# Optimization experiments

Hardware: AMD Instinct MI355X
Metric: run time of the kernel (lower is better)

The kernel has to match this reference:

```python
import jax, jax.numpy as jnp
import numpy as np

V, E, H, L, B, T = 32000, 512, 512, 4, 32, 64

def setup_inputs() -> dict:
    key = jax.random.key(0)
    ks = jax.random.split(key, 12)
    s = 0.04  # ~1/sqrt(H), matches torch LSTMCell uniform scale magnitude
    emb = jax.random.normal(ks[0], (V, E), jnp.float32) * s
    emb = emb.at[0].set(0.0)  # padding_idx=0
    return {
        'context': jax.random.normal(ks[1], (B, T, H), jnp.float32),
        'dec_input': jax.random.randint(ks[2], (B, T), 0, V),
        'h0': jax.random.normal(ks[3], (L, B, H), jnp.float32) * s,
        'c0': jax.random.normal(ks[4], (L, B, H), jnp.float32) * s,
        'emb': emb,
        'W_ih': jax.random.normal(ks[5], (L, 4 * H, E), jnp.float32) * s,
        'W_hh': jax.random.normal(ks[6], (L, 4 * H, H), jnp.float32) * s,
        'b_ih': jax.random.normal(ks[7], (L, 4 * H), jnp.float32) * s,
        'b_hh': jax.random.normal(ks[8], (L, 4 * H), jnp.float32) * s,
        'W_cls': jax.random.normal(ks[9], (V, H), jnp.float32) * s,
        'b_cls': jax.random.normal(ks[10], (V,), jnp.float32) * s,
    }

def _stack_lstm_scan(x, h0, c0, W_ih, W_hh, b_ih, b_hh):
    # x: [B,T,E] -> scan over time with L stacked LSTMCells + residual
    n_layers = W_ih.shape[0]

    def step(carry, x_t):
        h, c = carry  # each [L,B,H]
        inp = x_t
        new_h, new_c = [], []
        for i in range(n_layers):
            gates = inp @ W_ih[i].T + b_ih[i] + h[i] @ W_hh[i].T + b_hh[i]
            ig, fg, gg, og = jnp.split(gates, 4, axis=-1)  # torch order: i,f,g,o
            ci = jax.nn.sigmoid(fg) * c[i] + jax.nn.sigmoid(ig) * jnp.tanh(gg)
            hi = jax.nn.sigmoid(og) * jnp.tanh(ci)
            # residual when dims match (E == H here)
            inp = hi + inp if inp.shape[-1] == hi.shape[-1] else hi
            new_h.append(hi)
            new_c.append(ci)
        return (jnp.stack(new_h), jnp.stack(new_c)), inp

    (hT, cT), outs = jax.lax.scan(step, (h0, c0), jnp.swapaxes(x, 0, 1))
    return jnp.swapaxes(outs, 0, 1), hT, cT  # [B,T,H]

def reference(context, dec_input, h0, c0, emb, W_ih, W_hh, b_ih, b_hh, W_cls, b_cls):
    x = emb[dec_input]  # [B,T,E]; dropouts are identity (p=0 / eval)
    outs, hT, cT = _stack_lstm_scan(x, h0, c0, W_ih, W_hh, b_ih, b_hh)
    logits = outs @ W_cls.T + b_cls  # [B,T,V]
    # original applies log_softmax over dim=1 (the sequence dim) - faithful
    out = jax.nn.log_softmax(logits, axis=1)
    return (out, hT, cT)
```

## Files before the change

kernel.cpp:

```cpp
#include <hip/hip_runtime.h>
#include <math.h>

#define VOCAB 32000
#define HDIM  512
#define NLAYERS 4
#define BATCH 32
#define TSTEPS 64
typedef unsigned long long ULL;

typedef __attribute__((ext_vector_type(8))) short bf16x8;
typedef __attribute__((ext_vector_type(4))) float f32x4;

static __device__ __forceinline__ unsigned short f2b(float f) {
    union { float f; unsigned u; } v; v.f = f;
    return (unsigned short)((v.u + 0x7FFFu + ((v.u >> 16) & 1u)) >> 16);
}
static __device__ __forceinline__ float sigf(float x) { return 1.0f / (1.0f + __expf(-x)); }

static __device__ __forceinline__ int apack_off(int m, int k) {
    int k0 = k >> 5, mi = m >> 4;
    int lane = (m & 15) | (((k >> 3) & 3) << 4);
    return ((k0 * 2 + mi) * 64 + lane) * 8 + (k & 7);
}

__global__ void k_prep_w(const float* __restrict__ W_ih, const float* __restrict__ W_hh,
                         unsigned short* __restrict__ wp) {
    const int total = NLAYERS * 64 * 2 * 32 * 64 * 8;
    for (int idx = blockIdx.x * blockDim.x + threadIdx.x; idx < total;
         idx += gridDim.x * blockDim.x) {
        int sub = idx & 7, lane = (idx >> 3) & 63, k0 = (idx >> 9) & 31;
        int ni = (idx >> 14) & 1, bi = (idx >> 15) & 63, l = idx >> 21;
        int r = ni * 16 + (lane & 15);
        int k = k0 * 32 + ((lane >> 4) << 3) + sub;
        int j = (r & 3) * 512 + bi * 8 + (r >> 2);
        float v = (k < 512) ? W_ih[((size_t)l * 2048 + j) * 512 + k]
                            : W_hh[((size_t)l * 2048 + j) * 512 + (k - 512)];
        wp[idx] = f2b(v);
    }
}

__global__ void k_prep_bias(const float* __restrict__ b_ih, const float* __restrict__ b_hh,
                            float* __restrict__ bs) {
    int idx = blockIdx.x * blockDim.x + threadIdx.x;
    if (idx < NLAYERS * 64 * 32) {
        int r = idx & 31, bi = (idx >> 5) & 63, l = idx >> 11;
        int j = (r & 3) * 512 + bi * 8 + (r >> 2);
        bs[idx] = b_ih[l * 2048 + j] + b_hh[l * 2048 + j];
    }
}

__global__ void k_prep_wcls(const float* __restrict__ W_cls, unsigned short* __restrict__ wp) {
    int idx8 = blockIdx.x * blockDim.x + threadIdx.x;
    int lane = idx8 & 63, k0 = (idx8 >> 6) & 15, ni = (idx8 >> 10) & 1;
    int w = (idx8 >> 11) & 3, vt = idx8 >> 13;
    int v = vt * 128 + w * 32 + ni * 16 + (lane & 15);
    int kb = k0 * 32 + ((lane >> 4) << 3);
    const float* src = W_cls + (size_t)v * 512 + kb;
    float4 f0 = *(const float4*)(src);
    float4 f1 = *(const float4*)(src + 4);
    bf16x8 u;
    u[0] = (short)f2b(f0.x); u[1] = (short)f2b(f0.y);
    u[2] = (short)f2b(f0.z); u[3] = (short)f2b(f0.w);
    u[4] = (short)f2b(f1.x); u[5] = (short)f2b(f1.y);
    u[6] = (short)f2b(f1.z); u[7] = (short)f2b(f1.w);
    *(bf16x8*)(wp + (size_t)idx8 * 8) = u;
}

__global__ void k_embed(const float* __restrict__ emb, const int* __restrict__ dec,
                        float* __restrict__ seqF, unsigned short* __restrict__ seqBp) {
    int t = blockIdx.x;
    for (int i = threadIdx.x; i < BATCH * HDIM; i += blockDim.x) {
        int b = i >> 9, e = i & 511;
        int tok = dec[b * TSTEPS + t];
        float v = emb[(size_t)tok * HDIM + e];
        seqF[((size_t)t * BATCH + b) * HDIM + e] = v;
        seqBp[(size_t)t * 16384 + apack_off(b, e)] = f2b(v);
    }
}

__global__ void k_inith(const float* __restrict__ h0, unsigned short* __restrict__ apack) {
    int idx = blockIdx.x * blockDim.x + threadIdx.x;
    int l = idx >> 14, b = (idx >> 9) & 31, d = idx & 511;
    apack[(size_t)(l * 2) * 32768 + apack_off(b, 512 + d)] =
        f2b(h0[((size_t)l * BATCH + b) * HDIM + d]);
}

__global__ __launch_bounds__(256, 1) void k_lstm(
    unsigned short* apack,
    const unsigned short* __restrict__ wpack,
    const float* __restrict__ bsum,
    const unsigned short* __restrict__ seqBp,
    const float* __restrict__ seqF,
    float* outF,
    unsigned short* __restrict__ seqOut,
    const float* __restrict__ c0,
    float* __restrict__ outHT, float* __restrict__ outCT,
    unsigned* flags) {
    const int l = blockIdx.x >> 6, bi = blockIdx.x & 63;
    const int wave = threadIdx.x >> 6, lane = threadIdx.x & 63;
    const int mi = wave >> 1, ni = wave & 1;
    const int cb = threadIdx.x >> 3, dsl = threadIdx.x & 7;
    const int d = bi * 8 + dsl;

    __shared__ short sW[32768];
    __shared__ short sA[32768];
    __shared__ float sG[1024];
    __shared__ short sHexH[512];
    __shared__ short sHexO[512];

    {
        const unsigned short* wp = wpack + (size_t)blockIdx.x * 32768;
        #pragma unroll
        for (int i = 0; i < 16; ++i) {
            int off = (i * 256 + threadIdx.x) * 8;
            *(bf16x8*)(sW + off) = *(const bf16x8*)(wp + off);
        }
    }
    float4 bias = *(const float4*)(bsum + blockIdx.x * 32 + dsl * 4);
    float c = c0[((size_t)l * BATCH + cb) * HDIM + d];

    unsigned short* A0 = apack + (size_t)(l * 2 + 0) * 32768;
    unsigned short* A1 = apack + (size_t)(l * 2 + 1) * 32768;

    for (int t = 0; t < TSTEPS; ++t) {
        if (wave == 0 && t > 0) {
            const unsigned* fp = flags + (l * 64 + lane) * 16;
            while (__hip_atomic_load(fp, __ATOMIC_RELAXED, __HIP_MEMORY_SCOPE_AGENT)
                   < (unsigned)t)
                __builtin_amdgcn_s_sleep(1);
        }
        if (wave == 1 && l > 0) {
            const unsigned* fp = flags + ((l - 1) * 64 + lane) * 16;
            while (__hip_atomic_load(fp, __ATOMIC_RELAXED, __HIP_MEMORY_SCOPE_AGENT)
                   < (unsigned)(t + 1))
                __builtin_amdgcn_s_sleep(1);
        }
        if (wave == 2 && l < 3 && t > 0) {
            const unsigned* fp = flags + ((l + 1) * 64 + lane) * 16;
            while (__hip_atomic_load(fp, __ATOMIC_RELAXED, __HIP_MEMORY_SCOPE_AGENT)
                   < (unsigned)(t - 1))
                __builtin_amdgcn_s_sleep(1);
        }
        __syncthreads();

        float inpf;
        if (l == 0) inpf = seqF[((size_t)t * BATCH + cb) * HDIM + d];
        else inpf = __hip_atomic_load(&outF[(size_t)((l * 2 + (t & 1)) * BATCH + cb) * HDIM + d],
                                      __ATOMIC_RELAXED, __HIP_MEMORY_SCOPE_AGENT);

        const unsigned short* Ab = (t & 1) ? A1 : A0;
        const ULL* Abu = (const ULL*)Ab;
        ULL* sAu = (ULL*)sA;
        if (l == 0) {
            const unsigned short* sp = seqBp + (size_t)t * 16384;
            #pragma unroll
            for (int i = 0; i < 8; ++i) {
                int off = (i * 256 + threadIdx.x) * 8;
                *(bf16x8*)(sA + off) = *(const bf16x8*)(sp + off);
            }
            ULL tmp[16];
            #pragma unroll
            for (int i = 0; i < 16; ++i)
                tmp[i] = __hip_atomic_load(&Abu[(16 + i) * 256 + threadIdx.x],
                                           __ATOMIC_RELAXED, __HIP_MEMORY_SCOPE_AGENT);
            #pragma unroll
            for (int i = 0; i < 16; ++i)
                sAu[(16 + i) * 256 + threadIdx.x] = tmp[i];
        } else {
            ULL tmp[32];
            #pragma unroll
            for (int i = 0; i < 32; ++i)
                tmp[i] = __hip_atomic_load(&Abu[i * 256 + threadIdx.x],
                                           __ATOMIC_RELAXED, __HIP_MEMORY_SCOPE_AGENT);
            #pragma unroll
            for (int i = 0; i < 32; ++i)
                sAu[i * 256 + threadIdx.x] = tmp[i];
        }
        __syncthreads();

        f32x4 acc = {0.f, 0.f, 0.f, 0.f};
        const short* abase = sA + mi * 512 + lane * 8;
        const short* wbase = sW + ni * 16384 + lane * 8;
        #pragma unroll
        for (int k0 = 0; k0 < 32; ++k0)
            acc = __builtin_amdgcn_mfma_f32_16x16x32_bf16(
                *(const bf16x8*)(abase + k0 * 1024),
                *(const bf16x8*)(wbase + k0 * 512), acc, 0, 0, 0);

        int gb = mi * 16 + (lane >> 4) * 4;
        int gr = ni * 16 + (lane & 15);
        #pragma unroll
        for (int r = 0; r < 4; ++r) sG[(gb + r) * 32 + gr] = acc[r];
        __syncthreads();

        float4 g4 = *(const float4*)(sG + cb * 32 + dsl * 4);
        float gi = g4.x + bias.x, gf = g4.y + bias.y;
        float gg = g4.z + bias.z, go = g4.w + bias.w;
        float ci = sigf(gf) * c + sigf(gi) * tanhf(gg);
        float hi = sigf(go) * tanhf(ci);
        c = ci;
        float o = hi + inpf;

        sHexH[cb * 8 + dsl] = f2b(hi);
        sHexO[cb * 8 + dsl] = f2b(o);
        if (l < 3)
            __hip_atomic_store(&outF[(size_t)(((l + 1) * 2 + (t & 1)) * BATCH + cb) * HDIM + d],
                               o, __ATOMIC_RELAXED, __HIP_MEMORY_SCOPE_AGENT);
        if (t == TSTEPS - 1) {
            outHT[((size_t)l * BATCH + cb) * HDIM + d] = hi;
            outCT[((size_t)l * BATCH + cb) * HDIM + d] = ci;
        }
        __syncthreads();

        unsigned short* An = ((t + 1) & 1) ? A1 : A0;
        int i = threadIdx.x & 63, cbe = i >> 1, jh = i & 1;
        int lanecode = ((cbe & 15) | ((bi & 3) << 4)) * 2 + jh;
        if (threadIdx.x < 64) {
            int hoff = ((16 + (bi >> 2)) * 2 + (cbe >> 4)) * 128 + lanecode;
            __hip_atomic_store(&((ULL*)An)[hoff], ((const ULL*)sHexH)[i],
                               __ATOMIC_RELAXED, __HIP_MEMORY_SCOPE_AGENT);
        } else if (threadIdx.x < 128) {
            if (l < 3) {
                unsigned short* Anx = apack + (size_t)((l + 1) * 2 + (t & 1)) * 32768;
                int ooff = ((bi >> 2) * 2 + (cbe >> 4)) * 128 + lanecode;
                __hip_atomic_store(&((ULL*)Anx)[ooff], ((const ULL*)sHexO)[i],
                                   __ATOMIC_RELAXED, __HIP_MEMORY_SCOPE_AGENT);
            } else {
                int ulidx = ((((cbe * 16 + (bi >> 2)) * 4 + (t >> 4)) * 64 +
                             ((t & 15) | ((bi & 3) << 4))) * 2) + jh;
                ((ULL*)seqOut)[ulidx] = ((const ULL*)sHexO)[i];
            }
        }

        asm volatile("s_waitcnt vmcnt(0)" ::: "memory");
        __syncthreads();
        if (threadIdx.x == 0)
            __hip_atomic_store(&flags[(l * 64 + bi) * 16], (unsigned)(t + 1),
                               __ATOMIC_RELAXED, __HIP_MEMORY_SCOPE_AGENT);
    }
}

__global__ __launch_bounds__(256) void k_cls(
    const unsigned short* __restrict__ Ap,
    const unsigned short* __restrict__ Wp,
    float* __restrict__ out) {
    int b = blockIdx.x & 31;
    int vt = blockIdx.x >> 5;
    int wave = threadIdx.x >> 6;
    int lane = threadIdx.x & 63;

    __shared__ float sL[64 * 132];

    const unsigned short* abase = Ap + (size_t)b * 32768 + lane * 8;
    const unsigned short* wbase = Wp + (size_t)(vt * 4 + wave) * 16384 + lane * 8;

    f32x4 acc[4][2];
    #pragma unroll
    for (int i = 0; i < 4; ++i)
        #pragma unroll
        for (int j = 0; j < 2; ++j) acc[i][j] = (f32x4)(0.0f);

    #pragma unroll 4
    for (int k0 = 0; k0 < 16; ++k0) {
        bf16x8 a[4], bb[2];
        #pragma unroll
        for (int mi = 0; mi < 4; ++mi)
            a[mi] = *(const bf16x8*)(abase + (k0 * 4 + mi) * 512);
        #pragma unroll
        for (int ni = 0; ni < 2; ++ni)
            bb[ni] = *(const bf16x8*)(wbase + ni * 8192 + k0 * 512);
        #pragma unroll
        for (int mi = 0; mi < 4; ++mi)
            #pragma unroll
            for (int ni = 0; ni < 2; ++ni)
                acc[mi][ni] = __builtin_amdgcn_mfma_f32_16x16x32_bf16(a[mi], bb[ni], acc[mi][ni], 0, 0, 0);
    }

    #pragma unroll
    for (int ni = 0; ni < 2; ++ni) {
        float m = -1e30f;
        #pragma unroll
        for (int mi = 0; mi < 4; ++mi)
            #pragma unroll
            for (int r = 0; r < 4; ++r) m = fmaxf(m, acc[mi][ni][r]);
        m = fmaxf(m, __shfl_xor(m, 16));
        m = fmaxf(m, __shfl_xor(m, 32));
        float s = 0.f;
        #pragma unroll
        for (int mi = 0; mi < 4; ++mi)
            #pragma unroll
            for (int r = 0; r < 4; ++r) s += expf(acc[mi][ni][r] - m);
        s += __shfl_xor(s, 16);
        s += __shfl_xor(s, 32);
        float logZ = m + logf(s);
        int col = wave * 32 + ni * 16 + (lane & 15);
        #pragma unroll
        for (int mi = 0; mi < 4; ++mi) {
            #pragma unroll
            for (int r = 0; r < 4; ++r) {
                int row = mi * 16 + (lane >> 4) * 4 + r;
                sL[row * 132 + col] = acc[mi][ni][r] - logZ;
            }
        }
    }
    __syncthreads();

    float* obase = out + (size_t)b * TSTEPS * VOCAB + vt * 128;
    #pragma unroll
    for (int it = 0; it < 8; ++it) {
        int idx = it * 256 + threadIdx.x;
        int row = idx >> 5, c4 = (idx & 31) * 4;
        float4 val = *(const float4*)(sL + row * 132 + c4);
        *(float4*)(obase + (size_t)row * VOCAB + c4) = val;
    }
}

extern "C" void kernel_launch(void* const* d_in, const int* in_sizes, int n_in,
                              void* d_out, int out_size, void* d_ws, size_t ws_size,
                              hipStream_t stream) {
    const int*   dec   = (const int*)d_in[1];
    const float* h0    = (const float*)d_in[2];
    const float* c0    = (const float*)d_in[3];
    const float* emb   = (const float*)d_in[4];
    const float* W_ih  = (const float*)d_in[5];
    const float* W_hh  = (const float*)d_in[6];
    const float* b_ih  = (const float*)d_in[7];
    const float* b_hh  = (const float*)d_in[8];
    const float* W_cls = (const float*)d_in[9];

    const int LBH = NLAYERS * BATCH * HDIM;
    const size_t BTV = (size_t)BATCH * TSTEPS * VOCAB;

    char* ws = (char*)d_ws;
    size_t off = 0;
    auto alloc = [&](size_t bytes) -> void* {
        void* p = ws + off;
        off = (off + bytes + 255) & ~(size_t)255;
        return p;
    };
    unsigned short* wpack  = (unsigned short*)alloc((size_t)NLAYERS * 64 * 2 * 32 * 64 * 8 * 2);
    float*          bsum   = (float*)alloc((size_t)NLAYERS * 64 * 32 * 4);
    unsigned short* wpackC = (unsigned short*)alloc((size_t)VOCAB * HDIM * 2);
    float*          seqF   = (float*)alloc((size_t)TSTEPS * BATCH * HDIM * 4);
    unsigned short* seqBp  = (unsigned short*)alloc((size_t)TSTEPS * 16384 * 2);
    unsigned short* apack  = (unsigned short*)alloc((size_t)NLAYERS * 2 * 32768 * 2);
    float*          outF   = (float*)alloc((size_t)NLAYERS * 2 * BATCH * HDIM * 4);
    unsigned short* apackC = (unsigned short*)alloc((size_t)TSTEPS * BATCH * HDIM * 2);
    unsigned*       flags  = (unsigned*)alloc(16384);

    k_prep_w<<<4096, 256, 0, stream>>>(W_ih, W_hh, wpack);
    k_prep_bias<<<32, 256, 0, stream>>>(b_ih, b_hh, bsum);
    k_prep_wcls<<<8000, 256, 0, stream>>>(W_cls, wpackC);
    k_embed<<<TSTEPS, 256, 0, stream>>>(emb, dec, seqF, seqBp);
    k_inith<<<256, 256, 0, stream>>>(h0, apack);
    hipMemsetAsync(flags, 0, 16384, stream);

    k_lstm<<<256, 256, 0, stream>>>(apack, wpack, bsum, seqBp, seqF, outF, apackC,
                                    c0,
                                    (float*)d_out + BTV,
                                    (float*)d_out + BTV + LBH,
                                    flags);

    k_cls<<<250 * 32, 256, 0, stream>>>(apackC, wpackC, (float*)d_out);
}
```

Baseline: 499.3 us.

## Streamline LSTM cross-block sync with packed flags and 16-byte coherent transfers

```diff
diff --git a/kernel.cpp b/kernel.cpp
--- a/kernel.cpp
+++ b/kernel.cpp
@@ -10,12 +10,25 @@
 
 typedef __attribute__((ext_vector_type(8))) short bf16x8;
 typedef __attribute__((ext_vector_type(4))) float f32x4;
+typedef __attribute__((ext_vector_type(4))) unsigned int u32x4;
 
 static __device__ __forceinline__ unsigned short f2b(float f) {
     union { float f; unsigned u; } v; v.f = f;
     return (unsigned short)((v.u + 0x7FFFu + ((v.u >> 16) & 1u)) >> 16);
 }
 static __device__ __forceinline__ float sigf(float x) { return 1.0f / (1.0f + __expf(-x)); }
+
+static __device__ __forceinline__ u32x4 load16cp(const void* p) {
+    u32x4 r;
+    asm volatile("global_load_dwordx4 %0, %1, off sc0 sc1" : "=v"(r) : "v"(p) : "memory");
+    return r;
+}
+static __device__ __forceinline__ void store16cp(void* p, u32x4 v) {
+    asm volatile("global_store_dwordx4 %0, %1, off sc0 sc1" :: "v"(p), "v"(v) : "memory");
+}
+static __device__ __forceinline__ void waitvm0() {
+    asm volatile("s_waitcnt vmcnt(0)" ::: "memory");
+}
 
 static __device__ __forceinline__ int apack_off(int m, int k) {
     int k0 = k >> 5, mi = m >> 4;
@@ -102,11 +115,11 @@
     const int cb = threadIdx.x >> 3, dsl = threadIdx.x & 7;
     const int d = bi * 8 + dsl;
 
-    __shared__ short sW[32768];
-    __shared__ short sA[32768];
-    __shared__ float sG[1024];
-    __shared__ short sHexH[512];
-    __shared__ short sHexO[512];
+    __shared__ __align__(16) short sW[32768];
+    __shared__ __align__(16) short sA[32768];
+    __shared__ __align__(16) float sG[1024];
+    __shared__ __align__(16) short sHexH[256];
+    __shared__ __align__(16) short sHexO[256];
 
     {
         const unsigned short* wp = wpack + (size_t)blockIdx.x * 32768;
@@ -123,58 +136,58 @@
     unsigned short* A1 = apack + (size_t)(l * 2 + 1) * 32768;
 
     for (int t = 0; t < TSTEPS; ++t) {
-        if (wave == 0 && t > 0) {
-            const unsigned* fp = flags + (l * 64 + lane) * 16;
-            while (__hip_atomic_load(fp, __ATOMIC_RELAXED, __HIP_MEMORY_SCOPE_AGENT)
-                   < (unsigned)t)
+        if (l == 0) {
+            const u32x4* sp = (const u32x4*)(seqBp + (size_t)t * 16384);
+            u32x4* dA = (u32x4*)sA;
+            #pragma unroll
+            for (int i = 0; i < 8; ++i)
+                dA[i * 256 + threadIdx.x] = sp[i * 256 + threadIdx.x];
+        }
+
+        if (threadIdx.x < 64) {
+            unsigned n0 = (unsigned)t;
+            unsigned n1 = (unsigned)(t + 1);
+            unsigned n2 = (unsigned)(t > 0 ? t - 1 : 0);
+            const unsigned* f0 = flags + l * 64 + lane;
+            for (;;) {
+                unsigned v0 = __hip_atomic_load(f0, __ATOMIC_RELAXED, __HIP_MEMORY_SCOPE_AGENT);
+                unsigned v1 = (l > 0) ? __hip_atomic_load(f0 - 64, __ATOMIC_RELAXED,
+                                                          __HIP_MEMORY_SCOPE_AGENT) : 0xFFFFFFFFu;
+                unsigned v2 = (l < 3) ? __hip_atomic_load(f0 + 64, __ATOMIC_RELAXED,
+                                                          __HIP_MEMORY_SCOPE_AGENT) : 0xFFFFFFFFu;
+                if (v0 >= n0 && v1 >= n1 && v2 >= n2) break;
                 __builtin_amdgcn_s_sleep(1);
-        }
-        if (wave == 1 && l > 0) {
-            const unsigned* fp = flags + ((l - 1) * 64 + lane) * 16;
-            while (__hip_atomic_load(fp, __ATOMIC_RELAXED, __HIP_MEMORY_SCOPE_AGENT)
-                   < (unsigned)(t + 1))
-                __builtin_amdgcn_s_sleep(1);
-        }
-        if (wave == 2 && l < 3 && t > 0) {
-            const unsigned* fp = flags + ((l + 1) * 64 + lane) * 16;
-            while (__hip_atomic_load(fp, __ATOMIC_RELAXED, __HIP_MEMORY_SCOPE_AGENT)
-                   < (unsigned)(t - 1))
-                __builtin_amdgcn_s_sleep(1);
+            }
         }
         __syncthreads();
 
         float inpf;
         if (l == 0) inpf = seqF[((size_t)t * BATCH + cb) * HDIM + d];
-        else inpf = __hip_atomic_load(&outF[(size_t)((l * 2 + (t & 1)) * BATCH + cb) * HDIM + d],
+        else inpf = __hip_atomic_load(&outF[((size_t)(l * 2 + (t & 1)) * 64 + bi) * 256 + threadIdx.x],
                                       __ATOMIC_RELAXED, __HIP_MEMORY_SCOPE_AGENT);
 
         const unsigned short* Ab = (t & 1) ? A1 : A0;
-        const ULL* Abu = (const ULL*)Ab;
-        ULL* sAu = (ULL*)sA;
-        if (l == 0) {
-            const unsigned short* sp = seqBp + (size_t)t * 16384;
-            #pragma unroll
-            for (int i = 0; i < 8; ++i) {
-                int off = (i * 256 + threadIdx.x) * 8;
-                *(bf16x8*)(sA + off) = *(const bf16x8*)(sp + off);
+        {
+            u32x4* dA = (u32x4*)sA;
+            if (l == 0) {
+                u32x4 tmp[8];
+                #pragma unroll
+                for (int i = 0; i < 8; ++i)
+                    tmp[i] = load16cp((const char*)Ab + ((8 + i) * 256 + threadIdx.x) * 16);
+                waitvm0();
+                #pragma unroll
+                for (int i = 0; i < 8; ++i)
+                    dA[(8 + i) * 256 + threadIdx.x] = tmp[i];
+            } else {
+                u32x4 tmp[16];
+                #pragma unroll
+                for (int i = 0; i < 16; ++i)
+                    tmp[i] = load16cp((const char*)Ab + (i * 256 + threadIdx.x) * 16);
+                waitvm0();
+                #pragma unroll
+                for (int i = 0; i < 16; ++i)
+                    dA[i * 256 + threadIdx.x] = tmp[i];
             }
-            ULL tmp[16];
-            #pragma unroll
-            for (int i = 0; i < 16; ++i)
-                tmp[i] = __hip_atomic_load(&Abu[(16 + i) * 256 + threadIdx.x],
-                                           __ATOMIC_RELAXED, __HIP_MEMORY_SCOPE_AGENT);
-            #pragma unroll
-            for (int i = 0; i < 16; ++i)
-                sAu[(16 + i) * 256 + threadIdx.x] = tmp[i];
-        } else {
-            ULL tmp[32];
-            #pragma unroll
-            for (int i = 0; i < 32; ++i)
-                tmp[i] = __hip_atomic_load(&Abu[i * 256 + threadIdx.x],
-                                           __ATOMIC_RELAXED, __HIP_MEMORY_SCOPE_AGENT);
-            #pragma unroll
-            for (int i = 0; i < 32; ++i)
-                sAu[i * 256 + threadIdx.x] = tmp[i];
         }
         __syncthreads();
 
@@ -201,10 +214,10 @@
         c = ci;
         float o = hi + inpf;
 
-        sHexH[cb * 8 + dsl] = f2b(hi);
-        sHexO[cb * 8 + dsl] = f2b(o);
+        sHexH[threadIdx.x] = f2b(hi);
+        sHexO[threadIdx.x] = f2b(o);
         if (l < 3)
-            __hip_atomic_store(&outF[(size_t)(((l + 1) * 2 + (t & 1)) * BATCH + cb) * HDIM + d],
+            __hip_atomic_store(&outF[((size_t)((l + 1) * 2 + (t & 1)) * 64 + bi) * 256 + threadIdx.x],
                                o, __ATOMIC_RELAXED, __HIP_MEMORY_SCOPE_AGENT);
         if (t == TSTEPS - 1) {
             outHT[((size_t)l * BATCH + cb) * HDIM + d] = hi;
@@ -213,29 +226,29 @@
         __syncthreads();
 
         unsigned short* An = ((t + 1) & 1) ? A1 : A0;
-        int i = threadIdx.x & 63, cbe = i >> 1, jh = i & 1;
-        int lanecode = ((cbe & 15) | ((bi & 3) << 4)) * 2 + jh;
-        if (threadIdx.x < 64) {
-            int hoff = ((16 + (bi >> 2)) * 2 + (cbe >> 4)) * 128 + lanecode;
-            __hip_atomic_store(&((ULL*)An)[hoff], ((const ULL*)sHexH)[i],
-                               __ATOMIC_RELAXED, __HIP_MEMORY_SCOPE_AGENT);
-        } else if (threadIdx.x < 128) {
+        int tid = threadIdx.x;
+        if (tid < 32) {
+            int X = (tid & 15) | ((bi & 3) << 4);
+            int chunk = (16 + (bi >> 2)) * 2 + (tid >> 4);
+            store16cp((char*)An + chunk * 1024 + X * 16, ((const u32x4*)sHexH)[tid]);
+        } else if (tid >= 64 && tid < 96) {
+            int t2 = tid - 64;
+            int X = (t2 & 15) | ((bi & 3) << 4);
             if (l < 3) {
                 unsigned short* Anx = apack + (size_t)((l + 1) * 2 + (t & 1)) * 32768;
-                int ooff = ((bi >> 2) * 2 + (cbe >> 4)) * 128 + lanecode;
-                __hip_atomic_store(&((ULL*)Anx)[ooff], ((const ULL*)sHexO)[i],
-                                   __ATOMIC_RELAXED, __HIP_MEMORY_SCOPE_AGENT);
+                int chunk = (bi >> 2) * 2 + (t2 >> 4);
+                store16cp((char*)Anx + chunk * 1024 + X * 16, ((const u32x4*)sHexO)[t2]);
             } else {
-                int ulidx = ((((cbe * 16 + (bi >> 2)) * 4 + (t >> 4)) * 64 +
-                             ((t & 15) | ((bi & 3) << 4))) * 2) + jh;
-                ((ULL*)seqOut)[ulidx] = ((const ULL*)sHexO)[i];
+                int idx16 = ((t2 * 16 + (bi >> 2)) * 4 + (t >> 4)) * 64 +
+                            ((t & 15) | ((bi & 3) << 4));
+                ((u32x4*)seqOut)[idx16] = ((const u32x4*)sHexO)[t2];
             }
         }
 
-        asm volatile("s_waitcnt vmcnt(0)" ::: "memory");
+        waitvm0();
         __syncthreads();
         if (threadIdx.x == 0)
-            __hip_atomic_store(&flags[(l * 64 + bi) * 16], (unsigned)(t + 1),
+            __hip_atomic_store(&flags[l * 64 + bi], (unsigned)(t + 1),
                                __ATOMIC_RELAXED, __HIP_MEMORY_SCOPE_AGENT);
     }
 }
@@ -344,16 +357,16 @@
     float*          seqF   = (float*)alloc((size_t)TSTEPS * BATCH * HDIM * 4);
     unsigned short* seqBp  = (unsigned short*)alloc((size_t)TSTEPS * 16384 * 2);
     unsigned short* apack  = (unsigned short*)alloc((size_t)NLAYERS * 2 * 32768 * 2);
-    float*          outF   = (float*)alloc((size_t)NLAYERS * 2 * BATCH * HDIM * 4);
+    float*          outF   = (float*)alloc((size_t)8 * 64 * 256 * 4);
     unsigned short* apackC = (unsigned short*)alloc((size_t)TSTEPS * BATCH * HDIM * 2);
-    unsigned*       flags  = (unsigned*)alloc(16384);
+    unsigned*       flags  = (unsigned*)alloc(1024);
 
     k_prep_w<<<4096, 256, 0, stream>>>(W_ih, W_hh, wpack);
     k_prep_bias<<<32, 256, 0, stream>>>(b_ih, b_hh, bsum);
     k_prep_wcls<<<8000, 256, 0, stream>>>(W_cls, wpackC);
     k_embed<<<TSTEPS, 256, 0, stream>>>(emb, dec, seqF, seqBp);
     k_inith<<<256, 256, 0, stream>>>(h0, apack);
-    hipMemsetAsync(flags, 0, 16384, stream);
+    hipMemsetAsync(flags, 0, 1024, stream);
 
     k_lstm<<<256, 256, 0, stream>>>(apack, wpack, bsum, seqBp, seqF, outF, apackC,
                                     c0,
```

Measured after the change: 596.9 us (median of 5 runs). 19.6% more time.
